# Optimization experiments

Hardware: AMD Instinct MI355X
Metric: run time of the kernel (lower is better)

## Reference

```python
import jax, jax.numpy as jnp
import numpy as np

E = 100000      # number of edges
MUL = 64        # multiplicity of each irrep (0e and 1o)
DIM = MUL * 1 + MUL * 3  # 256 feature dim for 64x0e + 64x1o

INV_SQRT3 = 1.0 / np.sqrt(3.0)          # wigner-3j value for (0,1,1) and (1,1,0) paths
ALPHA0 = 1.0 / np.sqrt(2.0 * MUL * MUL)  # path norm: 2 paths feed the 0e output
ALPHA1 = 1.0 / np.sqrt(2.0 * MUL * MUL)  # path norm: 2 paths feed the 1o output


def _split(t):
    # t: [E, 256] -> scalars [E, MUL], vectors [E, MUL, 3]
    s = t[:, :MUL]
    v = t[:, MUL:].reshape(-1, MUL, 3)
    return s, v


def fc_tensor_product(x, y, W000, W110, W011, W101):
    """FullyConnectedTensorProduct(64x0e+64x1o, 64x0e+64x1o -> 64x0e+64x1o).

    Paths (uvw-connected, one weight [MUL,MUL,MUL] each):
      (0e,0e)->0e : cg = 1
      (1o,1o)->0e : cg = delta_ij / sqrt(3)
      (0e,1o)->1o : cg = delta_jk / sqrt(3)
      (1o,0e)->1o : cg = delta_ik / sqrt(3)
    """
    x0, x1 = _split(x)
    y0, y1 = _split(y)
    out0 = ALPHA0 * (
        jnp.einsum('eu,ev,uvw->ew', x0, y0, W000)
        + INV_SQRT3 * jnp.einsum('eui,evi,uvw->ew', x1, y1, W110)
    )
    out1 = ALPHA1 * INV_SQRT3 * (
        jnp.einsum('eu,evi,uvw->ewi', x0, y1, W011)
        + jnp.einsum('eui,ev,uvw->ewi', x1, y0, W101)
    )
    return jnp.concatenate([out0, out1.reshape(-1, MUL * 3)], axis=1)


def setup_inputs() -> dict:
    key = jax.random.key(0)
    ks = jax.random.split(key, 12)
    mk = lambda k, shape: jax.random.normal(k, shape, dtype=jnp.float32)
    return {
        'e1x': mk(ks[0], (E, DIM)),
        'e1y': mk(ks[1], (E, DIM)),
        'e2x': mk(ks[2], (E, DIM)),
        'e2y': mk(ks[3], (E, DIM)),
        'W1_000': mk(ks[4], (MUL, MUL, MUL)),
        'W1_110': mk(ks[5], (MUL, MUL, MUL)),
        'W1_011': mk(ks[6], (MUL, MUL, MUL)),
        'W1_101': mk(ks[7], (MUL, MUL, MUL)),
        'W2_000': mk(ks[8], (MUL, MUL, MUL)),
        'W2_110': mk(ks[9], (MUL, MUL, MUL)),
        'W2_011': mk(ks[10], (MUL, MUL, MUL)),
        'W2_101': mk(ks[11], (MUL, MUL, MUL)),
    }


def reference(e1x, e1y, e2x, e2y,
              W1_000, W1_110, W1_011, W1_101,
              W2_000, W2_110, W2_011, W2_101) -> jnp.ndarray:
    # SimpleEdgeBlock.forward: sum of one fully-connected TP per input tuple
    out = fc_tensor_product(e1x, e1y, W1_000, W1_110, W1_011, W1_101)
    out = out + fc_tensor_product(e2x, e2y, W2_000, W2_110, W2_011, W2_101)
    return out
```

## Files before the change

### kernel.cpp

```cpp
#include <hip/hip_runtime.h>
#include <stdint.h>


typedef __attribute__((ext_vector_type(8))) short short8;
typedef __attribute__((ext_vector_type(16))) float f32x16;
typedef unsigned short u16;

#define ETOT 100000

__device__ __forceinline__ unsigned pk2(float lo, float hi) {
  return __builtin_amdgcn_perm(__builtin_bit_cast(unsigned, hi),
                               __builtin_bit_cast(unsigned, lo), 0x07060302u);
}
__device__ __forceinline__ float bf2f(u16 s) {
  return __builtin_bit_cast(float, ((unsigned)s) << 16);
}
__device__ __forceinline__ void unpk8(short8 s, float f[8]) {
  uint4 u = __builtin_bit_cast(uint4, s);
  unsigned a[4] = {u.x, u.y, u.z, u.w};
#pragma unroll
  for (int jj = 0; jj < 4; ++jj) {
    f[2 * jj]     = __builtin_bit_cast(float, a[jj] << 16);
    f[2 * jj + 1] = __builtin_bit_cast(float, a[jj] & 0xffff0000u);
  }
}
__device__ __forceinline__ short8 scalepack(const float f[8], float ysc) {
  unsigned p0 = pk2(f[0] * ysc, f[1] * ysc);
  unsigned p1 = pk2(f[2] * ysc, f[3] * ysc);
  unsigned p2 = pk2(f[4] * ysc, f[5] * ysc);
  unsigned p3 = pk2(f[6] * ysc, f[7] * ysc);
  uint4 r = make_uint4(p0, p1, p2, p3);
  return __builtin_bit_cast(short8, r);
}
__device__ __forceinline__ short8 pack8(const float f[8]) {
  unsigned p0 = pk2(f[0], f[1]);
  unsigned p1 = pk2(f[2], f[3]);
  unsigned p2 = pk2(f[4], f[5]);
  unsigned p3 = pk2(f[6], f[7]);
  uint4 r = make_uint4(p0, p1, p2, p3);
  return __builtin_bit_cast(short8, r);
}

__global__ void prep_B(const float* __restrict__ W10, const float* __restrict__ W11,
                       const float* __restrict__ W12, const float* __restrict__ W13,
                       const float* __restrict__ W20, const float* __restrict__ W21,
                       const float* __restrict__ W22, const float* __restrict__ W23,
                       u16* __restrict__ B) {
  int idx = blockIdx.x * 256 + threadIdx.x;
  int k = idx & 16383;
  int w = (idx >> 14) & 63;
  int t = idx >> 20;
  int p = k >> 13;
  int half = (k >> 12) & 1;
  int v = (k >> 6) & 63;
  int u = k & 63;
  const float a0 = 0.011048543456039806f;
  const float a0s3 = a0 * 0.5773502691896258f;
  const float* Wsrc;
  float scale;
  if (t == 0) {
    Wsrc = half ? (p ? W21 : W11) : (p ? W20 : W10);
    scale = half ? a0s3 : a0;
  } else {
    Wsrc = half ? (p ? W23 : W13) : (p ? W22 : W12);
    scale = a0s3;
  }
  float val = Wsrc[u * 4096 + v * 64 + w] * scale;
  unsigned ub = __builtin_bit_cast(unsigned, val);
  ub += 0x7fffu + ((ub >> 16) & 1u);
  B[idx] = (u16)(ub >> 16);
}

__global__ __launch_bounds__(128, 2)
void tp_main(const float* __restrict__ e1x, const float* __restrict__ e1y,
             const float* __restrict__ e2x, const float* __restrict__ e2y,
             const u16* __restrict__ B, float* __restrict__ out) {
  __shared__ u16 ylds[4 * 64 * 64];
  __shared__ u16 blds[2][2 * 4 * 64 * 8];

  const int tid = threadIdx.x;
  const int wave = tid >> 6;
  const int lane = tid & 63;
  const int m = lane & 31;
  const int hw = lane >> 5;
  const int be0 = blockIdx.x * 64;
  const int e0 = be0 + wave * 32;
  const bool active = (e0 < ETOT);
  const int e = e0 + m;

  f32x16 acc[4][2] = {};
  short8 xc[4][4];

  int buf = 0;
#pragma unroll 1
  for (int p = 0; p < 2; ++p) {
    const float* X = p ? e2x : e1x;
    const float* Y = p ? e2y : e1y;
    __syncthreads();

#pragma unroll 4
    for (int n = 0; n < 32; ++n) {
      int flat4 = n * 128 + tid;
      int r = flat4 >> 6;
      int c4 = flat4 & 63;
      if (be0 + r < ETOT) {
        float4 v4 = *(const float4*)(Y + (size_t)(be0 + r) * 256 + c4 * 4);
        float vv[4] = {v4.x, v4.y, v4.z, v4.w};
#pragma unroll
        for (int kk = 0; kk < 4; ++kk) {
          int d = c4 * 4 + kk;
          int ch, vi;
          if (d < 64) { ch = 0; vi = d; }
          else { int dd = d - 64; ch = 1 + dd % 3; vi = dd / 3; }
          ylds[(ch * 64 + vi) * 64 + r] =
              (u16)(__builtin_bit_cast(unsigned, vv[kk]) >> 16);
        }
      }
    }

    if (active) {
#pragma unroll
      for (int q = 0; q < 4; ++q) {
        const float* px = X + (size_t)e * 256 + q * 16 + hw * 8;
        float4 a4 = *(const float4*)px;
        float4 b4 = *(const float4*)(px + 4);
        float f[8] = {a4.x, a4.y, a4.z, a4.w, b4.x, b4.y, b4.z, b4.w};
        xc[0][q] = pack8(f);
      }
#pragma unroll
      for (int i = 0; i < 3; ++i) {
        const float* px = X + (size_t)e * 256 + 64 + i;
#pragma unroll
        for (int q = 0; q < 4; ++q) {
          float f[8];
#pragma unroll
          for (int j = 0; j < 8; ++j) f[j] = px[(q * 16 + hw * 8 + j) * 3];
          xc[1 + i][q] = pack8(f);
        }
      }
    }

    auto stageB = [&](int kk0, int dstbuf) {
#pragma unroll
      for (int q = 0; q < 4; ++q) {
        int flat = q * 128 + tid;
        int t = flat >> 8;
        int kq = (flat >> 6) & 3;
        int w = flat & 63;
        const uint4* g = (const uint4*)(B + (size_t)(t * 64 + w) * 16384 +
                                        p * 8192 + kk0 + kq * 8);
        *(uint4*)&blds[dstbuf][flat * 8] = *g;
      }
    };

    stageB(0, buf);
    __syncthreads();

#pragma unroll 1
    for (int s = 0; s < 256; ++s) {
      if (s < 255) stageB((s + 1) * 32, buf ^ 1);
      if (active) {
        const u16* bb = blds[buf];
#pragma unroll
        for (int ksub = 0; ksub < 2; ++ksub) {
          int kk = s * 32 + ksub * 16;
          int half = kk >> 12;
          int lv = (kk >> 6) & 63;
          int qx = (kk >> 4) & 3;
          float ys[4];
#pragma unroll
          for (int ch = 0; ch < 4; ++ch)
            ys[ch] = bf2f(ylds[(ch * 64 + lv) * 64 + wave * 32 + m]);
          short8 bfrag[2][2];
#pragma unroll
          for (int tb = 0; tb < 2; ++tb)
#pragma unroll
            for (int n = 0; n < 2; ++n) {
              int slot = tb * 256 + (ksub * 2 + hw) * 64 + n * 32 + m;
              bfrag[tb][n] = *(const short8*)&bb[slot * 8];
            }
          short8 af[4];
          if (half == 0) {
            float xf[8];
            unpk8(xc[0][qx], xf);
            af[0] = scalepack(xf, ys[0]);
            af[1] = scalepack(xf, ys[1]);
            af[2] = scalepack(xf, ys[2]);
            af[3] = scalepack(xf, ys[3]);
          } else {
            float x0f[8], x1f[8], x2f[8];
            unpk8(xc[1][qx], x0f);
            unpk8(xc[2][qx], x1f);
            unpk8(xc[3][qx], x2f);
            float z[8];
#pragma unroll
            for (int j = 0; j < 8; ++j)
              z[j] = x0f[j] * ys[1] + x1f[j] * ys[2] + x2f[j] * ys[3];
            af[0] = pack8(z);
            af[1] = scalepack(x0f, ys[0]);
            af[2] = scalepack(x1f, ys[0]);
            af[3] = scalepack(x2f, ys[0]);
          }
#pragma unroll
          for (int t = 0; t < 4; ++t) {
            const int tb = t ? 1 : 0;
            acc[t][0] = __builtin_amdgcn_mfma_f32_32x32x16_bf16(
                af[t], bfrag[tb][0], acc[t][0], 0, 0, 0);
            acc[t][1] = __builtin_amdgcn_mfma_f32_32x32x16_bf16(
                af[t], bfrag[tb][1], acc[t][1], 0, 0, 0);
          }
        }
      }
      __syncthreads();
      buf ^= 1;
    }
  }

  if (active) {
#pragma unroll
    for (int t = 0; t < 4; ++t)
#pragma unroll
      for (int n0 = 0; n0 < 2; ++n0) {
        f32x16 c = acc[t][n0];
        int n = n0 * 32 + m;
#pragma unroll
        for (int r = 0; r < 16; ++r) {
          int row = (r & 3) + 8 * (r >> 2) + 4 * hw;
          int ee = e0 + row;
          size_t off;
          if (t == 0) off = (size_t)ee * 256 + n;
          else        off = (size_t)ee * 256 + 64 + n * 3 + (t - 1);
          out[off] = c[r];
        }
      }
  }
}

extern "C" void kernel_launch(void* const* d_in, const int* in_sizes, int n_in,
                              void* d_out, int out_size, void* d_ws, size_t ws_size,
                              hipStream_t stream) {
  const float* e1x = (const float*)d_in[0];
  const float* e1y = (const float*)d_in[1];
  const float* e2x = (const float*)d_in[2];
  const float* e2y = (const float*)d_in[3];
  const size_t bElems = (size_t)2 * 64 * 16384;
  if (ws_size < bElems * sizeof(u16)) return;
  u16* B = (u16*)d_ws;
  prep_B<<<8192, 256, 0, stream>>>(
      (const float*)d_in[4], (const float*)d_in[5], (const float*)d_in[6],
      (const float*)d_in[7], (const float*)d_in[8], (const float*)d_in[9],
      (const float*)d_in[10], (const float*)d_in[11], B);
  tp_main<<<(ETOT + 63) / 64, 128, 0, stream>>>(e1x, e1y, e2x, e2y, B,
                                                (float*)d_out);
}
```

Before: 2.885 ms.

## Split output columns across 4 waves, restage B via direct global-to-LDS loads

```diff
diff --git a/kernel.cpp b/kernel.cpp
--- a/kernel.cpp
+++ b/kernel.cpp
@@ -5,6 +5,7 @@
 typedef __attribute__((ext_vector_type(8))) short short8;
 typedef __attribute__((ext_vector_type(16))) float f32x16;
 typedef unsigned short u16;
+typedef unsigned int u32;
 
 #define ETOT 100000
 
@@ -47,11 +48,14 @@
                        const float* __restrict__ W22, const float* __restrict__ W23,
                        u16* __restrict__ B) {
   int idx = blockIdx.x * 256 + threadIdx.x;
-  int k = idx & 16383;
-  int w = (idx >> 14) & 63;
-  int t = idx >> 20;
-  int p = k >> 13;
-  int half = (k >> 12) & 1;
+  int j = idx & 7;
+  int w = (idx >> 3) & 63;
+  int oct = (idx >> 9) & 3;
+  int s = (idx >> 11) & 255;
+  int p = (idx >> 19) & 1;
+  int t = (idx >> 20) & 1;
+  int k = s * 32 + oct * 8 + j;
+  int half = k >> 12;
   int v = (k >> 6) & 63;
   int u = k & 63;
   const float a0 = 0.011048543456039806f;
@@ -71,25 +75,42 @@
   B[idx] = (u16)(ub >> 16);
 }
 
-__global__ __launch_bounds__(128, 2)
+__global__ __launch_bounds__(256, 3)
 void tp_main(const float* __restrict__ e1x, const float* __restrict__ e1y,
              const float* __restrict__ e2x, const float* __restrict__ e2y,
              const u16* __restrict__ B, float* __restrict__ out) {
-  __shared__ u16 ylds[4 * 64 * 64];
-  __shared__ u16 blds[2][2 * 4 * 64 * 8];
+  __shared__ u16 ylds[64 * 64 * 4];
+  __shared__ u16 blds[2][4096];
 
   const int tid = threadIdx.x;
   const int wave = tid >> 6;
   const int lane = tid & 63;
   const int m = lane & 31;
   const int hw = lane >> 5;
+  const int we = wave & 1;
+  const int wn = wave >> 1;
   const int be0 = blockIdx.x * 64;
-  const int e0 = be0 + wave * 32;
+  const int e0 = be0 + we * 32;
   const bool active = (e0 < ETOT);
   const int e = e0 + m;
 
-  f32x16 acc[4][2] = {};
+  f32x16 acc[4] = {};
   short8 xc[4][4];
+
+  const int lfrag = (hw * 64 + wn * 32 + m) * 8;
+  const int yrow = (we * 32 + m) * 4;
+
+  auto stage = [&](int p, int s, int dstbuf) {
+#pragma unroll
+    for (int q = 0; q < 2; ++q) {
+      size_t g = ((size_t)((q * 2 + p) * 256 + s)) * 2048 + (size_t)tid * 8;
+      int flat = q * 256 + tid;
+      __builtin_amdgcn_global_load_lds(
+          (const __attribute__((address_space(1))) u32*)(B + g),
+          (__attribute__((address_space(3))) u32*)(&blds[dstbuf][flat * 8]),
+          16, 0, 0);
+    }
+  };
 
   int buf = 0;
 #pragma unroll 1
@@ -99,8 +120,8 @@
     __syncthreads();
 
 #pragma unroll 4
-    for (int n = 0; n < 32; ++n) {
-      int flat4 = n * 128 + tid;
+    for (int n = 0; n < 16; ++n) {
+      int flat4 = n * 256 + tid;
       int r = flat4 >> 6;
       int c4 = flat4 & 63;
       if (be0 + r < ETOT) {
@@ -112,7 +133,7 @@
           int ch, vi;
           if (d < 64) { ch = 0; vi = d; }
           else { int dd = d - 64; ch = 1 + dd % 3; vi = dd / 3; }
-          ylds[(ch * 64 + vi) * 64 + r] =
+          ylds[vi * 256 + r * 4 + ch] =
               (u16)(__builtin_bit_cast(unsigned, vv[kk]) >> 16);
         }
       }
@@ -140,53 +161,33 @@
       }
     }
 
-    auto stageB = [&](int kk0, int dstbuf) {
-#pragma unroll
-      for (int q = 0; q < 4; ++q) {
-        int flat = q * 128 + tid;
-        int t = flat >> 8;
-        int kq = (flat >> 6) & 3;
-        int w = flat & 63;
-        const uint4* g = (const uint4*)(B + (size_t)(t * 64 + w) * 16384 +
-                                        p * 8192 + kk0 + kq * 8);
-        *(uint4*)&blds[dstbuf][flat * 8] = *g;
-      }
-    };
-
-    stageB(0, buf);
+    stage(p, 0, buf);
     __syncthreads();
 
 #pragma unroll 1
     for (int s = 0; s < 256; ++s) {
-      if (s < 255) stageB((s + 1) * 32, buf ^ 1);
+      if (s < 255) stage(p, s + 1, buf ^ 1);
       if (active) {
         const u16* bb = blds[buf];
+        const int half = s >> 7;
+        const int lv = (s >> 1) & 63;
+        const int uh = s & 1;
+        ushort4 y4 = *(const ushort4*)&ylds[lv * 256 + yrow];
+        float ys0 = bf2f(y4.x), ys1 = bf2f(y4.y);
+        float ys2 = bf2f(y4.z), ys3 = bf2f(y4.w);
 #pragma unroll
         for (int ksub = 0; ksub < 2; ++ksub) {
-          int kk = s * 32 + ksub * 16;
-          int half = kk >> 12;
-          int lv = (kk >> 6) & 63;
-          int qx = (kk >> 4) & 3;
-          float ys[4];
-#pragma unroll
-          for (int ch = 0; ch < 4; ++ch)
-            ys[ch] = bf2f(ylds[(ch * 64 + lv) * 64 + wave * 32 + m]);
-          short8 bfrag[2][2];
-#pragma unroll
-          for (int tb = 0; tb < 2; ++tb)
-#pragma unroll
-            for (int n = 0; n < 2; ++n) {
-              int slot = tb * 256 + (ksub * 2 + hw) * 64 + n * 32 + m;
-              bfrag[tb][n] = *(const short8*)&bb[slot * 8];
-            }
+          int qx = uh * 2 + ksub;
+          short8 bf0 = *(const short8*)&bb[ksub * 1024 + lfrag];
+          short8 bf1 = *(const short8*)&bb[2048 + ksub * 1024 + lfrag];
           short8 af[4];
           if (half == 0) {
             float xf[8];
             unpk8(xc[0][qx], xf);
-            af[0] = scalepack(xf, ys[0]);
-            af[1] = scalepack(xf, ys[1]);
-            af[2] = scalepack(xf, ys[2]);
-            af[3] = scalepack(xf, ys[3]);
+            af[0] = scalepack(xf, ys0);
+            af[1] = scalepack(xf, ys1);
+            af[2] = scalepack(xf, ys2);
+            af[3] = scalepack(xf, ys3);
           } else {
             float x0f[8], x1f[8], x2f[8];
             unpk8(xc[1][qx], x0f);
@@ -195,20 +196,16 @@
             float z[8];
 #pragma unroll
             for (int j = 0; j < 8; ++j)
-              z[j] = x0f[j] * ys[1] + x1f[j] * ys[2] + x2f[j] * ys[3];
+              z[j] = x0f[j] * ys1 + x1f[j] * ys2 + x2f[j] * ys3;
             af[0] = pack8(z);
-            af[1] = scalepack(x0f, ys[0]);
-            af[2] = scalepack(x1f, ys[0]);
-            af[3] = scalepack(x2f, ys[0]);
+            af[1] = scalepack(x0f, ys0);
+            af[2] = scalepack(x1f, ys0);
+            af[3] = scalepack(x2f, ys0);
           }
-#pragma unroll
-          for (int t = 0; t < 4; ++t) {
-            const int tb = t ? 1 : 0;
-            acc[t][0] = __builtin_amdgcn_mfma_f32_32x32x16_bf16(
-                af[t], bfrag[tb][0], acc[t][0], 0, 0, 0);
-            acc[t][1] = __builtin_amdgcn_mfma_f32_32x32x16_bf16(
-                af[t], bfrag[tb][1], acc[t][1], 0, 0, 0);
-          }
+          acc[0] = __builtin_amdgcn_mfma_f32_32x32x16_bf16(af[0], bf0, acc[0], 0, 0, 0);
+          acc[1] = __builtin_amdgcn_mfma_f32_32x32x16_bf16(af[1], bf1, acc[1], 0, 0, 0);
+          acc[2] = __builtin_amdgcn_mfma_f32_32x32x16_bf16(af[2], bf1, acc[2], 0, 0, 0);
+          acc[3] = __builtin_amdgcn_mfma_f32_32x32x16_bf16(af[3], bf1, acc[3], 0, 0, 0);
         }
       }
       __syncthreads();
@@ -217,22 +214,20 @@
   }
 
   if (active) {
-#pragma unroll
-    for (int t = 0; t < 4; ++t)
-#pragma unroll
-      for (int n0 = 0; n0 < 2; ++n0) {
-        f32x16 c = acc[t][n0];
-        int n = n0 * 32 + m;
-#pragma unroll
-        for (int r = 0; r < 16; ++r) {
-          int row = (r & 3) + 8 * (r >> 2) + 4 * hw;
-          int ee = e0 + row;
-          size_t off;
-          if (t == 0) off = (size_t)ee * 256 + n;
-          else        off = (size_t)ee * 256 + 64 + n * 3 + (t - 1);
-          out[off] = c[r];
-        }
-      }
+    const int n = wn * 32 + m;
+#pragma unroll
+    for (int t = 0; t < 4; ++t) {
+      f32x16 c = acc[t];
+#pragma unroll
+      for (int r = 0; r < 16; ++r) {
+        int row = (r & 3) + 8 * (r >> 2) + 4 * hw;
+        int ee = e0 + row;
+        size_t off;
+        if (t == 0) off = (size_t)ee * 256 + n;
+        else        off = (size_t)ee * 256 + 64 + n * 3 + (t - 1);
+        out[off] = c[r];
+      }
+    }
   }
 }
 
@@ -250,6 +245,6 @@
       (const float*)d_in[4], (const float*)d_in[5], (const float*)d_in[6],
       (const float*)d_in[7], (const float*)d_in[8], (const float*)d_in[9],
       (const float*)d_in[10], (const float*)d_in[11], B);
-  tp_main<<<(ETOT + 63) / 64, 128, 0, stream>>>(e1x, e1y, e2x, e2y, B,
+  tp_main<<<(ETOT + 63) / 64, 256, 0, stream>>>(e1x, e1y, e2x, e2y, B,
                                                 (float*)d_out);
 }
```

New measurement: 2.923 ms. Within noise of the previous version (+1.3%).
